# Kernel optimization log

Hardware: AMD Instinct MI355X
Metric: run time of the kernel (lower is better)

The kernel has to match this reference:

```python
import jax, jax.numpy as jnp
import numpy as np

IN_FEATURES = 128
OUT_FEATURES = 64
NUM_HEADS = 4
NEGATIVE_SLOPE = 0.2


def setup_inputs() -> dict:
    key = jax.random.key(0)
    k1, k2, k3, k4 = jax.random.split(key, 4)
    B, N = 2, 4096
    inputs = jax.random.normal(k1, (B, N, IN_FEATURES), dtype=jnp.float32)
    # glorot-style scales
    s_w = (6.0 / (IN_FEATURES + OUT_FEATURES * NUM_HEADS)) ** 0.5
    s_a = (6.0 / (OUT_FEATURES + 1)) ** 0.5
    W = jax.random.uniform(k2, (IN_FEATURES, OUT_FEATURES * NUM_HEADS), jnp.float32, -s_w, s_w)
    a_src = jax.random.uniform(k3, (NUM_HEADS, OUT_FEATURES, 1), jnp.float32, -s_a, s_a)
    a_dst = jax.random.uniform(k4, (NUM_HEADS, OUT_FEATURES, 1), jnp.float32, -s_a, s_a)
    bias = jnp.zeros((OUT_FEATURES * NUM_HEADS,), dtype=jnp.float32)
    return {"inputs": inputs, "W": W, "a_src": a_src, "a_dst": a_dst, "bias": bias}


def reference(inputs, W, a_src, a_dst, bias):
    B, N, _ = inputs.shape
    H, D = a_src.shape[0], a_src.shape[1]
    # project and split heads: [B, H, N, D]
    h = jnp.matmul(inputs, W).reshape(B, N, H, D).transpose(0, 2, 1, 3)
    # additive attention scalars per node per head
    e_src = jnp.einsum('bhnd,hd->bhn', h, a_src[..., 0])  # a_src^T (W h_i)
    e_dst = jnp.einsum('bhnd,hd->bhn', h, a_dst[..., 0])  # a_dst^T (W h_j)
    # e[b,h,i,j] = e_src[b,h,i] + e_dst[b,h,j]  (matches e_src + e_dst^T in TF code)
    e = e_src[:, :, :, None] + e_dst[:, :, None, :]
    e = jnp.where(e > 0, e, NEGATIVE_SLOPE * e)  # leaky_relu
    alpha = jax.nn.softmax(e, axis=-1)  # softmax over neighbors j
    # weighted sum of values: [B, H, N, D]
    out = jnp.einsum('bhij,bhjd->bhid', alpha, h)
    out = out.transpose(0, 2, 1, 3).reshape(B, N, H * D)  # concat heads
    out = out + bias
    return jax.nn.elu(out)
```

## Files before the change

kernel.cpp:

```cpp
#include <hip/hip_runtime.h>
#include <hip/hip_fp16.h>
#include <math.h>

#define NH 4
#define DD 64
#define NF 256
#define KF 128
#define NN 4096
#define NB 2
#define NG 8
#define CH 32
#define NCH 128
#define SUB 8

typedef _Float16 h8_t __attribute__((ext_vector_type(8)));
typedef float f4_t __attribute__((ext_vector_type(4)));

__global__ __launch_bounds__(256) void k_gemm(const float* __restrict__ X,
                                              const float* __restrict__ W,
                                              const float* __restrict__ a_src,
                                              const float* __restrict__ a_dst,
                                              __half* __restrict__ Hout,
                                              float* __restrict__ s_arr,
                                              float* __restrict__ d_arr) {
  __shared__ float As[64][132];
  __shared__ _Float16 WT[64][136];
  const int bm = blockIdx.x;
  const int bn = blockIdx.y;
  const int tid = threadIdx.x;

  for (int i = tid; i < 64 * 32; i += 256) {
    int r = i >> 5, c4 = i & 31;
    float4 v = *(const float4*)(X + ((size_t)(bm * 64 + r)) * KF + c4 * 4);
    *(float4*)&As[r][c4 * 4] = v;
  }
  for (int i = tid; i < 64 * 128; i += 256) {
    int k = i >> 6, c = i & 63;
    WT[c][k] = (_Float16)W[(size_t)k * NF + bn * 64 + c];
  }
  __syncthreads();

  const int lane = tid & 63, w = tid >> 6;
  const int l15 = lane & 15, lq = lane >> 4;

  f4_t acc[4] = {f4_t{0.f,0.f,0.f,0.f}, f4_t{0.f,0.f,0.f,0.f},
                 f4_t{0.f,0.f,0.f,0.f}, f4_t{0.f,0.f,0.f,0.f}};

  #pragma unroll
  for (int kk = 0; kk < 4; ++kk) {
    const int koff = kk * 32 + lq * 8;
    h8_t a;
    {
      const float* ap = &As[w * 16 + l15][koff];
      float4 x0 = *(const float4*)ap;
      float4 x1 = *(const float4*)(ap + 4);
      a[0] = (_Float16)x0.x; a[1] = (_Float16)x0.y;
      a[2] = (_Float16)x0.z; a[3] = (_Float16)x0.w;
      a[4] = (_Float16)x1.x; a[5] = (_Float16)x1.y;
      a[6] = (_Float16)x1.z; a[7] = (_Float16)x1.w;
    }
    #pragma unroll
    for (int t = 0; t < 4; ++t) {
      h8_t b = *(const h8_t*)&WT[t * 16 + l15][koff];
      acc[t] = __builtin_amdgcn_mfma_f32_16x16x32_f16(a, b, acc[t], 0, 0, 0);
    }
  }

  float asv[4], adv[4];
  #pragma unroll
  for (int t = 0; t < 4; ++t) {
    asv[t] = a_src[bn * 64 + t * 16 + l15];
    adv[t] = a_dst[bn * 64 + t * 16 + l15];
  }
  #pragma unroll
  for (int j = 0; j < 4; ++j) {
    const int grow = bm * 64 + w * 16 + lq * 4 + j;
    float ps = 0.f, pd = 0.f;
    #pragma unroll
    for (int t = 0; t < 4; ++t) {
      float hv = acc[t][j];
      Hout[(size_t)grow * NF + bn * 64 + t * 16 + l15] = __float2half(hv);
      ps += hv * asv[t];
      pd += hv * adv[t];
    }
    #pragma unroll
    for (int off = 1; off < 16; off <<= 1) {
      ps += __shfl_xor(ps, off);
      pd += __shfl_xor(pd, off);
    }
    if (l15 == 0) {
      int b = grow >> 12, n = grow & (NN - 1);
      int g = b * NH + bn;
      s_arr[g * NN + n] = ps;
      d_arr[g * NN + n] = pd;
    }
  }
}

__global__ __launch_bounds__(1024) void k_sort(const float* __restrict__ d_arr,
                                               const float* __restrict__ s_arr,
                                               float* __restrict__ dsort, int* __restrict__ dperm,
                                               float* __restrict__ tsort, int* __restrict__ tperm) {
  __shared__ uint4 skey[1024];
  __shared__ float vals[NN];
  const int bid = blockIdx.x;
  const bool isT = bid >= NG;
  const int g = isT ? bid - NG : bid;
  const float* src = isT ? s_arr : d_arr;
  float* okey = isT ? tsort : dsort;
  int* operm = isT ? tperm : dperm;
  const int tid = threadIdx.x;

  unsigned kk[4];
  {
    float4 v = *(const float4*)(src + g * NN + 4 * tid);
    float f[4] = {v.x, v.y, v.z, v.w};
    #pragma unroll
    for (int r = 0; r < 4; ++r) {
      float fv = isT ? -f[r] : f[r];
      vals[4 * tid + r] = fv;
      unsigned u = __float_as_uint(fv);
      u = (u & 0x80000000u) ? ~u : (u | 0x80000000u);
      kk[r] = (u & 0xFFFFF000u) | (unsigned)(4 * tid + r);
    }
  }

  #define CEU(a, b, asc)                                           \
    do { unsigned ka = kk[a], kb = kk[b];                          \
      unsigned mn = ka < kb ? ka : kb, mx = ka < kb ? kb : ka;     \
      kk[a] = (asc) ? mn : mx; kk[b] = (asc) ? mx : mn; } while (0)

  CEU(0, 1, true);
  CEU(2, 3, false);

  #pragma unroll
  for (int k = 4; k <= NN; k <<= 1) {
    const bool asc = (tid & (k >> 2)) == 0;
    #pragma unroll
    for (int j = k >> 1; j > 0; j >>= 1) {
      if (j >= 256) {
        const int tdist = j >> 2;
        skey[tid] = make_uint4(kk[0], kk[1], kk[2], kk[3]);
        __syncthreads();
        uint4 p = skey[tid ^ tdist];
        const bool lower = (tid & tdist) == 0;
        const bool keepMin = (lower == asc);
        #pragma unroll
        for (int r = 0; r < 4; ++r) {
          unsigned pk = (&p.x)[r];
          unsigned mn = kk[r] < pk ? kk[r] : pk;
          unsigned mx = kk[r] < pk ? pk : kk[r];
          kk[r] = keepMin ? mn : mx;
        }
        __syncthreads();
      } else if (j >= 4) {
        const int dist = j >> 2;
        const bool lower = (tid & dist) == 0;
        const bool keepMin = (lower == asc);
        #pragma unroll
        for (int r = 0; r < 4; ++r) {
          unsigned pk = (unsigned)__shfl_xor((int)kk[r], dist);
          unsigned mn = kk[r] < pk ? kk[r] : pk;
          unsigned mx = kk[r] < pk ? pk : kk[r];
          kk[r] = keepMin ? mn : mx;
        }
      } else if (j == 2) {
        CEU(0, 2, asc);
        CEU(1, 3, asc);
      } else {
        CEU(0, 1, asc);
        CEU(2, 3, asc);
      }
    }
  }
  #undef CEU

  __syncthreads();
  float4 ov;
  int4 op;
  #pragma unroll
  for (int r = 0; r < 4; ++r) {
    int idx = (int)(kk[r] & 0xFFFu);
    (&ov.x)[r] = vals[idx];
    (&op.x)[r] = idx;
  }
  *(float4*)(okey + g * NN + 4 * tid) = ov;
  *(int4*)(operm + g * NN + 4 * tid) = op;
}

__global__ __launch_bounds__(256) void k_part(const __half* __restrict__ Hmat,
                                              const float* __restrict__ dsort,
                                              const int* __restrict__ dperm,
                                              float* __restrict__ chunkP, float* __restrict__ chunkS,
                                              float* __restrict__ chunkPw, float* __restrict__ chunkSw) {
  __shared__ float subP[4][64], subS[4][64];
  __shared__ float subPw[4], subSw[4];
  const int ch = blockIdx.x;
  const int g = blockIdx.y;
  const int b = g >> 2, h = g & 3;
  const int c = threadIdx.x & 63;
  const int w = threadIdx.x >> 6;
  const int gNN = g * NN;
  const size_t bNN = (size_t)b * NN;
  const int h64 = h * 64;
  const float dmax = dsort[gNN + NN - 1];
  const int kw0 = ch * CH + w * SUB;

  int j8[SUB]; float d8[SUB], hv8[SUB];
  #pragma unroll
  for (int l = 0; l < SUB; ++l) j8[l] = dperm[gNN + kw0 + l];
  #pragma unroll
  for (int l = 0; l < SUB; ++l) d8[l] = dsort[gNN + kw0 + l];
  #pragma unroll
  for (int l = 0; l < SUB; ++l) hv8[l] = __half2float(Hmat[(bNN + j8[l]) * NF + h64 + c]);

  float pa = 0.f, sa = 0.f, pw = 0.f, sw = 0.f;
  #pragma unroll
  for (int l = 0; l < SUB; ++l) {
    float wp = __expf(0.2f * (d8[l] - dmax));
    float ws = __expf(d8[l] - dmax);
    pa += wp * hv8[l]; sa += ws * hv8[l]; pw += wp; sw += ws;
  }
  subP[w][c] = pa; subS[w][c] = sa;
  if (c == 0) { subPw[w] = pw; subSw[w] = sw; }
  __syncthreads();

  if (w == 0) {
    float tp = subP[0][c] + subP[1][c] + subP[2][c] + subP[3][c];
    float ts = subS[0][c] + subS[1][c] + subS[2][c] + subS[3][c];
    chunkP[(g * NCH + ch) * 64 + c] = tp;
    chunkS[(g * NCH + ch) * 64 + c] = ts;
    if (c == 0) {
      chunkPw[g * NCH + ch] = subPw[0] + subPw[1] + subPw[2] + subPw[3];
      chunkSw[g * NCH + ch] = subSw[0] + subSw[1] + subSw[2] + subSw[3];
    }
  }
}

__global__ __launch_bounds__(256, 4) void k_serve(const __half* __restrict__ Hmat,
                                                  const float* __restrict__ dsort,
                                                  const int* __restrict__ dperm,
                                                  const float* __restrict__ tsort,
                                                  const int* __restrict__ tperm,
                                                  const float* __restrict__ chunkP, const float* __restrict__ chunkS,
                                                  const float* __restrict__ chunkPw, const float* __restrict__ chunkSw,
                                                  const float* __restrict__ bias,
                                                  float* __restrict__ out) {
  __shared__ float PPloc[CH + 1][64], PSloc[CH + 1][64];
  __shared__ float ppwLoc[CH + 1], pswLoc[CH + 1];
  __shared__ float subP[4][64], subS[4][64], sall[4][64];
  __shared__ float subPw[4], subSw[4];

  const int ch = blockIdx.x & (NCH - 1);
  const int g = blockIdx.x >> 7;
  const int b = g >> 2, h = g & 3;
  const int c = threadIdx.x & 63;
  const int w = threadIdx.x >> 6;
  const int gNN = g * NN;
  const size_t bNN = (size_t)b * NN;
  const int h64 = h * 64;
  const float dmax = dsort[gNN + NN - 1];
  const int kw0 = ch * CH + w * SUB;

  int j8[SUB]; float d8[SUB], hv8[SUB];
  #pragma unroll
  for (int l = 0; l < SUB; ++l) j8[l] = dperm[gNN + kw0 + l];
  #pragma unroll
  for (int l = 0; l < SUB; ++l) d8[l] = dsort[gNN + kw0 + l];
  #pragma unroll
  for (int l = 0; l < SUB; ++l) hv8[l] = __half2float(Hmat[(bNN + j8[l]) * NF + h64 + c]);

  float ppv[SUB], psv[SUB], ppw[SUB], psw[SUB];
  {
    float ap = 0.f, as = 0.f, aw = 0.f, aswv = 0.f;
    #pragma unroll
    for (int l = 0; l < SUB; ++l) {
      float wp = __expf(0.2f * (d8[l] - dmax));
      float ws = __expf(d8[l] - dmax);
      ap += wp * hv8[l]; as += ws * hv8[l]; aw += wp; aswv += ws;
      ppv[l] = ap; psv[l] = as; ppw[l] = aw; psw[l] = aswv;
    }
    subP[w][c] = ap; subS[w][c] = as;
    if (c == 0) { subPw[w] = aw; subSw[w] = aswv; }
  }
  __syncthreads();

  {
    float oP = 0.f, oS = 0.f, oPw = 0.f, oSw = 0.f;
    #pragma unroll
    for (int t = 0; t < 4; ++t) {
      if (t < w) { oP += subP[t][c]; oS += subS[t][c]; oPw += subPw[t]; oSw += subSw[t]; }
    }
    #pragma unroll
    for (int l = 0; l < SUB; ++l) {
      PPloc[w * SUB + 1 + l][c] = ppv[l] + oP;
      PSloc[w * SUB + 1 + l][c] = psv[l] + oS;
    }
    if (c == 0) {
      #pragma unroll
      for (int l = 0; l < SUB; ++l) {
        ppwLoc[w * SUB + 1 + l] = ppw[l] + oPw;
        pswLoc[w * SUB + 1 + l] = psw[l] + oSw;
      }
    }
    if (w == 0) {
      PPloc[0][c] = 0.f; PSloc[0][c] = 0.f;
      if (c == 0) { ppwLoc[0] = 0.f; pswLoc[0] = 0.f; }
    }
  }
  __syncthreads();

  {
    float pp = 0.f, sp = 0.f, sa = 0.f;
    for (int t = w; t < ch; t += 4) pp += chunkP[(g * NCH + t) * 64 + c];
    for (int t = w; t < NCH; t += 4) {
      float v = chunkS[(g * NCH + t) * 64 + c];
      sa += v;
      if (t < ch) sp += v;
    }
    subP[w][c] = pp; subS[w][c] = sp; sall[w][c] = sa;
  }

  float offPw, offSw, totSw;
  {
    float w1 = chunkPw[g * NCH + c];
    float w2 = chunkPw[g * NCH + 64 + c];
    float pwo = (c < ch ? w1 : 0.f) + (c + 64 < ch ? w2 : 0.f);
    float u1 = chunkSw[g * NCH + c];
    float u2 = chunkSw[g * NCH + 64 + c];
    float swo = (c < ch ? u1 : 0.f) + (c + 64 < ch ? u2 : 0.f);
    float stw = u1 + u2;
    #pragma unroll
    for (int off = 1; off < 64; off <<= 1) {
      pwo += __shfl_xor(pwo, off);
      swo += __shfl_xor(swo, off);
      stw += __shfl_xor(stw, off);
    }
    offPw = pwo; offSw = swo; totSw = stw;
  }
  __syncthreads();

  const float offP = subP[0][c] + subP[1][c] + subP[2][c] + subP[3][c];
  const float offS = subS[0][c] + subS[1][c] + subS[2][c] + subS[3][c];
  const float totS = sall[0][c] + sall[1][c] + sall[2][c] + sall[3][c];

  const float* ts = tsort + gNN;
  int rlo, rhi;
  {
    float blo = dsort[gNN + ch * CH];
    if (ch == 0) rlo = 0;
    else {
      int lo = 0, hi = NN;
      while (lo < hi) { int mid = (lo + hi) >> 1; if (ts[mid] < blo) lo = mid + 1; else hi = mid; }
      rlo = lo;
    }
    if (ch == NCH - 1) rhi = NN;
    else {
      float bhi = dsort[gNN + (ch + 1) * CH];
      int lo = 0, hi = NN;
      while (lo < hi) { int mid = (lo + hi) >> 1; if (ts[mid] < bhi) lo = mid + 1; else hi = mid; }
      rhi = lo;
    }
  }

  const float myd = (c < 32) ? dsort[gNN + ch * CH + c] : __int_as_float(0x7f800000);
  const float biasv = bias[h64 + c];

  for (int r = rlo + w; r < rhi; r += 4) {
    const float t = ts[r];
    const int i = tperm[gNN + r];
    const int mloc = __popcll(__ballot(myd <= t));
    const float numB = PPloc[mloc][c] + offP;
    const float denB = ppwLoc[mloc] + offPw;
    const float numA = totS - (PSloc[mloc][c] + offS);
    const float denA = totSw - (pswLoc[mloc] + offSw);
    const float si = -t;
    const float sdm = si + dmax;
    const float mx = sdm > 0.f ? sdm : 0.2f * sdm;
    const float alpha = __expf(sdm - mx);
    const float beta = __expf(0.2f * sdm - mx);
    const float den = alpha * denA + beta * denB;
    float val = (alpha * numA + beta * numB) / den + biasv;
    float o = val > 0.f ? val : expm1f(val);
    out[(bNN + i) * NF + h64 + c] = o;
  }
}

extern "C" void kernel_launch(void* const* d_in, const int* in_sizes, int n_in,
                              void* d_out, int out_size, void* d_ws, size_t ws_size,
                              hipStream_t stream) {
  const float* X = (const float*)d_in[0];
  const float* W = (const float*)d_in[1];
  const float* a_src = (const float*)d_in[2];
  const float* a_dst = (const float*)d_in[3];
  const float* bias = (const float*)d_in[4];
  float* out = (float*)d_out;

  float* ws = (float*)d_ws;
  float* s_arr = ws;
  float* d_arr = s_arr + NG * NN;
  float* dsort = d_arr + NG * NN;
  int* dperm = (int*)(dsort + NG * NN);
  float* tsort = (float*)(dperm + NG * NN);
  int* tperm = (int*)(tsort + NG * NN);
  float* chunkP = (float*)(tperm + NG * NN);
  float* chunkS = chunkP + NG * NCH * 64;
  float* chunkPw = chunkS + NG * NCH * 64;
  float* chunkSw = chunkPw + NG * NCH;
  __half* Hmat = (__half*)(chunkSw + NG * NCH);

  k_gemm<<<dim3(128, 4), 256, 0, stream>>>(X, W, a_src, a_dst, Hmat, s_arr, d_arr);
  k_sort<<<2 * NG, 1024, 0, stream>>>(d_arr, s_arr, dsort, dperm, tsort, tperm);
  k_part<<<dim3(NCH, NG), 256, 0, stream>>>(Hmat, dsort, dperm, chunkP, chunkS, chunkPw, chunkSw);
  k_serve<<<NG * NCH, 256, 0, stream>>>(Hmat, dsort, dperm, tsort, tperm,
                                        chunkP, chunkS, chunkPw, chunkSw, bias, out);
}
```

Baseline: 61.56 us.

## Sort 8 keys per thread, derive exp via powers, replace binary search with ballots

The bitonic sort now runs 512 threads with 8 keys each. More compare-exchange stages happen in registers, and the shared-memory stages use a struct-of-arrays layout with fewer barriers. In the partial-sum kernels the second exponential is computed as the fifth power of the first, which replaces one exp per element with multiplies. The serial binary searches over the sorted source scores are replaced by a two-level wavefront ballot search. The sort now has less parallelism per block, and the power trick can change rounding slightly.

```diff
diff --git a/kernel.cpp b/kernel.cpp
--- a/kernel.cpp
+++ b/kernel.cpp
@@ -97,11 +97,11 @@
   }
 }
 
-__global__ __launch_bounds__(1024) void k_sort(const float* __restrict__ d_arr,
-                                               const float* __restrict__ s_arr,
-                                               float* __restrict__ dsort, int* __restrict__ dperm,
-                                               float* __restrict__ tsort, int* __restrict__ tperm) {
-  __shared__ uint4 skey[1024];
+__global__ __launch_bounds__(512) void k_sort(const float* __restrict__ d_arr,
+                                              const float* __restrict__ s_arr,
+                                              float* __restrict__ dsort, int* __restrict__ dperm,
+                                              float* __restrict__ tsort, int* __restrict__ tperm) {
+  __shared__ unsigned skey[8][512];
   __shared__ float vals[NN];
   const int bid = blockIdx.x;
   const bool isT = bid >= NG;
@@ -111,17 +111,18 @@
   int* operm = isT ? tperm : dperm;
   const int tid = threadIdx.x;
 
-  unsigned kk[4];
-  {
-    float4 v = *(const float4*)(src + g * NN + 4 * tid);
-    float f[4] = {v.x, v.y, v.z, v.w};
-    #pragma unroll
-    for (int r = 0; r < 4; ++r) {
+  unsigned kk[8];
+  {
+    float4 v0 = *(const float4*)(src + g * NN + 8 * tid);
+    float4 v1 = *(const float4*)(src + g * NN + 8 * tid + 4);
+    float f[8] = {v0.x, v0.y, v0.z, v0.w, v1.x, v1.y, v1.z, v1.w};
+    #pragma unroll
+    for (int r = 0; r < 8; ++r) {
       float fv = isT ? -f[r] : f[r];
-      vals[4 * tid + r] = fv;
+      vals[8 * tid + r] = fv;
       unsigned u = __float_as_uint(fv);
       u = (u & 0x80000000u) ? ~u : (u | 0x80000000u);
-      kk[r] = (u & 0xFFFFF000u) | (unsigned)(4 * tid + r);
+      kk[r] = (u & 0xFFFFF000u) | (unsigned)(8 * tid + r);
     }
   }
 
@@ -130,62 +131,61 @@
       unsigned mn = ka < kb ? ka : kb, mx = ka < kb ? kb : ka;     \
       kk[a] = (asc) ? mn : mx; kk[b] = (asc) ? mx : mn; } while (0)
 
-  CEU(0, 1, true);
-  CEU(2, 3, false);
-
-  #pragma unroll
-  for (int k = 4; k <= NN; k <<= 1) {
-    const bool asc = (tid & (k >> 2)) == 0;
+  CEU(0, 1, true); CEU(2, 3, false); CEU(4, 5, true); CEU(6, 7, false);
+  CEU(0, 2, true); CEU(1, 3, true); CEU(4, 6, false); CEU(5, 7, false);
+  CEU(0, 1, true); CEU(2, 3, true); CEU(4, 5, false); CEU(6, 7, false);
+
+  #pragma unroll
+  for (int k = 8; k <= NN; k <<= 1) {
+    const bool asc = (tid & (k >> 3)) == 0;
     #pragma unroll
     for (int j = k >> 1; j > 0; j >>= 1) {
-      if (j >= 256) {
-        const int tdist = j >> 2;
-        skey[tid] = make_uint4(kk[0], kk[1], kk[2], kk[3]);
+      if (j >= 512) {
+        const int tdist = j >> 3;
+        #pragma unroll
+        for (int r = 0; r < 8; ++r) skey[r][tid] = kk[r];
         __syncthreads();
-        uint4 p = skey[tid ^ tdist];
-        const bool lower = (tid & tdist) == 0;
-        const bool keepMin = (lower == asc);
+        const bool keepMin = ((tid & tdist) == 0) == asc;
         #pragma unroll
-        for (int r = 0; r < 4; ++r) {
-          unsigned pk = (&p.x)[r];
+        for (int r = 0; r < 8; ++r) {
+          unsigned pk = skey[r][tid ^ tdist];
           unsigned mn = kk[r] < pk ? kk[r] : pk;
           unsigned mx = kk[r] < pk ? pk : kk[r];
           kk[r] = keepMin ? mn : mx;
         }
         __syncthreads();
-      } else if (j >= 4) {
-        const int dist = j >> 2;
-        const bool lower = (tid & dist) == 0;
-        const bool keepMin = (lower == asc);
+      } else if (j >= 8) {
+        const int dist = j >> 3;
+        const bool keepMin = ((tid & dist) == 0) == asc;
         #pragma unroll
-        for (int r = 0; r < 4; ++r) {
+        for (int r = 0; r < 8; ++r) {
           unsigned pk = (unsigned)__shfl_xor((int)kk[r], dist);
           unsigned mn = kk[r] < pk ? kk[r] : pk;
           unsigned mx = kk[r] < pk ? pk : kk[r];
           kk[r] = keepMin ? mn : mx;
         }
+      } else if (j == 4) {
+        CEU(0, 4, asc); CEU(1, 5, asc); CEU(2, 6, asc); CEU(3, 7, asc);
       } else if (j == 2) {
-        CEU(0, 2, asc);
-        CEU(1, 3, asc);
+        CEU(0, 2, asc); CEU(1, 3, asc); CEU(4, 6, asc); CEU(5, 7, asc);
       } else {
-        CEU(0, 1, asc);
-        CEU(2, 3, asc);
+        CEU(0, 1, asc); CEU(2, 3, asc); CEU(4, 5, asc); CEU(6, 7, asc);
       }
     }
   }
   #undef CEU
 
-  __syncthreads();
-  float4 ov;
-  int4 op;
-  #pragma unroll
-  for (int r = 0; r < 4; ++r) {
+  float ov[8]; int op[8];
+  #pragma unroll
+  for (int r = 0; r < 8; ++r) {
     int idx = (int)(kk[r] & 0xFFFu);
-    (&ov.x)[r] = vals[idx];
-    (&op.x)[r] = idx;
-  }
-  *(float4*)(okey + g * NN + 4 * tid) = ov;
-  *(int4*)(operm + g * NN + 4 * tid) = op;
+    ov[r] = vals[idx];
+    op[r] = idx;
+  }
+  *(float4*)(okey + g * NN + 8 * tid)     = make_float4(ov[0], ov[1], ov[2], ov[3]);
+  *(float4*)(okey + g * NN + 8 * tid + 4) = make_float4(ov[4], ov[5], ov[6], ov[7]);
+  *(int4*)(operm + g * NN + 8 * tid)      = make_int4(op[0], op[1], op[2], op[3]);
+  *(int4*)(operm + g * NN + 8 * tid + 4)  = make_int4(op[4], op[5], op[6], op[7]);
 }
 
 __global__ __launch_bounds__(256) void k_part(const __half* __restrict__ Hmat,
@@ -218,7 +218,8 @@
   #pragma unroll
   for (int l = 0; l < SUB; ++l) {
     float wp = __expf(0.2f * (d8[l] - dmax));
-    float ws = __expf(d8[l] - dmax);
+    float w2 = wp * wp;
+    float ws = w2 * w2 * wp;
     pa += wp * hv8[l]; sa += ws * hv8[l]; pw += wp; sw += ws;
   }
   subP[w][c] = pa; subS[w][c] = sa;
@@ -276,7 +277,8 @@
     #pragma unroll
     for (int l = 0; l < SUB; ++l) {
       float wp = __expf(0.2f * (d8[l] - dmax));
-      float ws = __expf(d8[l] - dmax);
+      float w2 = wp * wp;
+      float ws = w2 * w2 * wp;
       ap += wp * hv8[l]; as += ws * hv8[l]; aw += wp; aswv += ws;
       ppv[l] = ap; psv[l] = as; ppw[l] = aw; psw[l] = aswv;
     }
@@ -347,19 +349,30 @@
   const float* ts = tsort + gNN;
   int rlo, rhi;
   {
-    float blo = dsort[gNN + ch * CH];
+    const float p1 = ts[c * 64 + 63];
     if (ch == 0) rlo = 0;
     else {
-      int lo = 0, hi = NN;
-      while (lo < hi) { int mid = (lo + hi) >> 1; if (ts[mid] < blo) lo = mid + 1; else hi = mid; }
-      rlo = lo;
+      const float blo = dsort[gNN + ch * CH];
+      unsigned long long m1 = __ballot(p1 < blo);
+      int blk = __popcll(m1);
+      if (blk == 64) rlo = NN;
+      else {
+        float p2 = ts[blk * 64 + c];
+        unsigned long long m2 = __ballot(p2 < blo);
+        rlo = blk * 64 + __popcll(m2);
+      }
     }
     if (ch == NCH - 1) rhi = NN;
     else {
-      float bhi = dsort[gNN + (ch + 1) * CH];
-      int lo = 0, hi = NN;
-      while (lo < hi) { int mid = (lo + hi) >> 1; if (ts[mid] < bhi) lo = mid + 1; else hi = mid; }
-      rhi = lo;
+      const float bhi = dsort[gNN + (ch + 1) * CH];
+      unsigned long long m1 = __ballot(p1 < bhi);
+      int blk = __popcll(m1);
+      if (blk == 64) rhi = NN;
+      else {
+        float p2 = ts[blk * 64 + c];
+        unsigned long long m2 = __ballot(p2 < bhi);
+        rhi = blk * 64 + __popcll(m2);
+      }
     }
   }
 
@@ -410,7 +423,7 @@
   __half* Hmat = (__half*)(chunkSw + NG * NCH);
 
   k_gemm<<<dim3(128, 4), 256, 0, stream>>>(X, W, a_src, a_dst, Hmat, s_arr, d_arr);
-  k_sort<<<2 * NG, 1024, 0, stream>>>(d_arr, s_arr, dsort, dperm, tsort, tperm);
+  k_sort<<<2 * NG, 512, 0, stream>>>(d_arr, s_arr, dsort, dperm, tsort, tperm);
   k_part<<<dim3(NCH, NG), 256, 0, stream>>>(Hmat, dsort, dperm, chunkP, chunkS, chunkPw, chunkSw);
   k_serve<<<NG * NCH, 256, 0, stream>>>(Hmat, dsort, dperm, tsort, tperm,
                                         chunkP, chunkS, chunkPw, chunkSw, bias, out);
```

Result: faster. 57.68 us (-6.3%).
